# Kernel optimization log

Measured on AMD Instinct MI355X. Metric: run time of the kernel, lower is better.

The kernel has to match this reference:

```python
import jax, jax.numpy as jnp
import numpy as np

KERNEL = 5
PAD = (KERNEL - 1) // 2  # fixed_padding with dilation=1: pad_beg = pad_end = 2


def setup_inputs() -> dict:
    key = jax.random.key(0)
    kx, kw = jax.random.split(key)
    x = jax.random.normal(kx, (4, 4, 1024, 1024), dtype=jnp.float32)
    weight = jax.random.normal(kw, (4, 4, KERNEL, KERNEL), dtype=jnp.float32)
    return {"x": x, "weight": weight}


def reference(x, weight):
    """Morphological dilation2d: out[b,o,h,w] = max_{c,i,j} (x_pad[b,c,h+i,w+j] + w[o,c,i,j]).

    Equivalent to the torch unfold + broadcast-add + max over dim C*k*k, but computed
    as a fused sliding-window max-plus without materializing the im2col tensor.
    """
    B, C, H, W = x.shape
    k = weight.shape[-1]
    xp = jnp.pad(x, ((0, 0), (0, 0), (PAD, PAD), (PAD, PAD)))  # zero pad, same as F.pad
    out = None
    for i in range(k):
        for j in range(k):
            patch = xp[:, :, i:i + H, j:j + W]          # (B, C, H, W)
            w_ij = weight[:, :, i, j]                    # (O, C)
            # max over in_channels of (x + w) for this tap
            val = jnp.max(patch[:, None] + w_ij[None, :, :, None, None], axis=2)  # (B, O, H, W)
            out = val if out is None else jnp.maximum(out, val)
    return out
```

## Files before the change

kernel.cpp:

```cpp
#include <hip/hip_runtime.h>


constexpr int Himg = 1024, Wimg = 1024, Cin = 4, Cout = 4, Kn = 5;
constexpr int TH = 8, TW = 128;
constexpr int LR = TH + 4;
constexpr int LC = TW + 8;
constexpr int LC4 = LC / 4;

typedef float v2f __attribute__((ext_vector_type(2)));

__global__ void reorg_w(const float* __restrict__ w, float* __restrict__ wt) {
  int idx = threadIdx.x;
  if (idx < Cout * Cin * Kn * Kn) {
    int o  = idx / (Cin * Kn * Kn);
    int r  = idx % (Cin * Kn * Kn);
    int c  = r / (Kn * Kn);
    int r2 = r % (Kn * Kn);
    int i  = r2 / Kn, j = r2 % Kn;
    wt[((c * Kn + i) * Kn + j) * Cout + o] = w[idx];
  }
}

__device__ __forceinline__ float max5(float a, float b, float c, float d, float e) {
  return fmaxf(fmaxf(a, b), fmaxf(c, fmaxf(d, e)));
}

template <bool TRANS>
__global__ __launch_bounds__(256) void morph(const float* __restrict__ x,
                                             const float* __restrict__ wt,
                                             float* __restrict__ out) {
  __shared__ __align__(16) float xs[Cin][LR][LC];
  const int tid = threadIdx.x;
  const int tile_w0 = blockIdx.x * TW;
  const int tile_r0 = blockIdx.y * TH;
  const int b = blockIdx.z;

  for (int idx = tid; idx < Cin * LR * LC4; idx += 256) {
    const int c   = idx / (LR * LC4);
    const int rem = idx - c * (LR * LC4);
    const int row = rem / LC4;
    const int ch  = rem - row * LC4;
    const int gr  = tile_r0 - 2 + row;
    const int gc  = tile_w0 - 4 + ch * 4;
    float4 v = make_float4(0.f, 0.f, 0.f, 0.f);
    if ((unsigned)gr < (unsigned)Himg) {
      const float* src = x + ((size_t)(b * Cin + c) * Himg + gr) * Wimg;
      if (gc >= 0 && gc <= Wimg - 4) {
        v = *(const float4*)(src + gc);
      } else {
        if ((unsigned)(gc + 0) < (unsigned)Wimg) v.x = src[gc + 0];
        if ((unsigned)(gc + 1) < (unsigned)Wimg) v.y = src[gc + 1];
        if ((unsigned)(gc + 2) < (unsigned)Wimg) v.z = src[gc + 2];
        if ((unsigned)(gc + 3) < (unsigned)Wimg) v.w = src[gc + 3];
      }
    }
    *(float4*)&xs[c][row][ch * 4] = v;
  }
  __syncthreads();

  const int tx = tid & 31;
  const int ty = tid >> 5;

  float acc[Cout][4];
#pragma unroll
  for (int o = 0; o < Cout; ++o)
#pragma unroll
    for (int p = 0; p < 4; ++p) acc[o][p] = -3.4e38f;

#define ACC_O(O, WA)                                                                     \
  do {                                                                                   \
    v2f p01[5], p23[5];                                                                  \
    _Pragma("unroll") for (int j = 0; j < 5; ++j) {                                      \
      v2f wb = {WA[j], WA[j]};                                                           \
      v2f a2 = {win[2 + j], win[3 + j]};                                                 \
      v2f b2 = {win[4 + j], win[5 + j]};                                                 \
      p01[j] = a2 + wb;                                                                  \
      p23[j] = b2 + wb;                                                                  \
    }                                                                                    \
    acc[O][0] = fmaxf(acc[O][0], max5(p01[0].x, p01[1].x, p01[2].x, p01[3].x, p01[4].x)); \
    acc[O][1] = fmaxf(acc[O][1], max5(p01[0].y, p01[1].y, p01[2].y, p01[3].y, p01[4].y)); \
    acc[O][2] = fmaxf(acc[O][2], max5(p23[0].x, p23[1].x, p23[2].x, p23[3].x, p23[4].x)); \
    acc[O][3] = fmaxf(acc[O][3], max5(p23[0].y, p23[1].y, p23[2].y, p23[3].y, p23[4].y)); \
  } while (0)

#pragma unroll 1
  for (int c = 0; c < Cin; ++c) {
#pragma unroll
    for (int i = 0; i < Kn; ++i) {
      const float* rowp = &xs[c][ty + i][tx * 4];
      float4 q0 = *(const float4*)(rowp);
      float4 q1 = *(const float4*)(rowp + 4);
      float4 q2 = *(const float4*)(rowp + 8);
      float win[12] = {q0.x, q0.y, q0.z, q0.w, q1.x, q1.y, q1.z, q1.w,
                       q2.x, q2.y, q2.z, q2.w};

      float wo0[5], wo1[5], wo2[5], wo3[5];
      if (TRANS) {
        const float4* wq = (const float4*)wt + (c * Kn + i) * Kn;
#pragma unroll
        for (int j = 0; j < Kn; ++j) {
          float4 wv = wq[j];
          wo0[j] = wv.x; wo1[j] = wv.y; wo2[j] = wv.z; wo3[j] = wv.w;
        }
      } else {
#pragma unroll
        for (int j = 0; j < Kn; ++j) {
          wo0[j] = wt[((0 * Cin + c) * Kn + i) * Kn + j];
          wo1[j] = wt[((1 * Cin + c) * Kn + i) * Kn + j];
          wo2[j] = wt[((2 * Cin + c) * Kn + i) * Kn + j];
          wo3[j] = wt[((3 * Cin + c) * Kn + i) * Kn + j];
        }
      }

      ACC_O(0, wo0);
      ACC_O(1, wo1);
      ACC_O(2, wo2);
      ACC_O(3, wo3);
    }
  }
#undef ACC_O

  const int r = tile_r0 + ty;
  const int gc0 = tile_w0 + tx * 4;
#pragma unroll
  for (int o = 0; o < Cout; ++o) {
    float4 res = make_float4(acc[o][0], acc[o][1], acc[o][2], acc[o][3]);
    *(float4*)&out[((size_t)(b * Cout + o) * Himg + r) * Wimg + gc0] = res;
  }
}

extern "C" void kernel_launch(void* const* d_in, const int* in_sizes, int n_in,
                              void* d_out, int out_size, void* d_ws, size_t ws_size,
                              hipStream_t stream) {
  const float* x = (const float*)d_in[0];
  const float* w = (const float*)d_in[1];
  float* out = (float*)d_out;

  dim3 grid(Wimg / TW, Himg / TH, 4);

  if (ws_size >= sizeof(float) * Cout * Cin * Kn * Kn) {
    float* wt = (float*)d_ws;
    reorg_w<<<dim3(1), dim3(512), 0, stream>>>(w, wt);
    morph<true><<<grid, dim3(256), 0, stream>>>(x, wt, out);
  } else {
    morph<false><<<grid, dim3(256), 0, stream>>>(x, w, out);
  }
}
```

Before: 154.3 us.

## Double-buffer channel tiles in LDS with register prefetch and packed v2f max-plus

Instead of loading all four input channels into LDS at once, the kernel stages one channel at a time in a double buffer and prefetches the next channel into registers while computing the current one. The tile grows to 16 rows, and each thread now computes 8 outputs split into interleaved pairs so the adds run as packed v2f operations. Weights are pre-duplicated into pairs and read through the constant address space. The goal is to overlap global loads with compute, cut LDS footprint and raise arithmetic density, at the cost of more syncs and strided LDS reads that may cause bank conflicts.

```diff
diff --git a/kernel.cpp b/kernel.cpp
--- a/kernel.cpp
+++ b/kernel.cpp
@@ -2,14 +2,16 @@
 
 
 constexpr int Himg = 1024, Wimg = 1024, Cin = 4, Cout = 4, Kn = 5;
-constexpr int TH = 8, TW = 128;
+constexpr int TH = 16, TW = 128;
 constexpr int LR = TH + 4;
-constexpr int LC = TW + 8;
-constexpr int LC4 = LC / 4;
+constexpr int LCU = TW + 12;
+constexpr int LC = 164;
+constexpr int NCH = LR * (LCU / 4);
 
 typedef float v2f __attribute__((ext_vector_type(2)));
+typedef const float __attribute__((address_space(4))) cfloat;
 
-__global__ void reorg_w(const float* __restrict__ w, float* __restrict__ wt) {
+__global__ void reorg_w(const float* __restrict__ w, float* __restrict__ wt2) {
   int idx = threadIdx.x;
   if (idx < Cout * Cin * Kn * Kn) {
     int o  = idx / (Cin * Kn * Kn);
@@ -17,115 +19,142 @@
     int c  = r / (Kn * Kn);
     int r2 = r % (Kn * Kn);
     int i  = r2 / Kn, j = r2 % Kn;
-    wt[((c * Kn + i) * Kn + j) * Cout + o] = w[idx];
+    float v = w[idx];
+    int dst = (((c * Kn + i) * Cout + o) * Kn + j) * 2;
+    wt2[dst + 0] = v;
+    wt2[dst + 1] = v;
   }
 }
 
-__device__ __forceinline__ float max5(float a, float b, float c, float d, float e) {
-  return fmaxf(fmaxf(a, b), fmaxf(c, fmaxf(d, e)));
-}
+template <bool FAST>
+__global__ __launch_bounds__(256) void morph(const float* __restrict__ x,
+                                             const float* __restrict__ wt2,
+                                             const float* __restrict__ wraw,
+                                             float* __restrict__ out) {
+  __shared__ __align__(16) float xs[2][LR][LC];
+  const int tid = threadIdx.x;
+  const int bw = blockIdx.x * TW;
+  const int br = blockIdx.y * TH;
+  const int b  = blockIdx.z;
+  const int tx = tid & 15;
+  const int ty = tid >> 4;
 
-template <bool TRANS>
-__global__ __launch_bounds__(256) void morph(const float* __restrict__ x,
-                                             const float* __restrict__ wt,
-                                             float* __restrict__ out) {
-  __shared__ __align__(16) float xs[Cin][LR][LC];
-  const int tid = threadIdx.x;
-  const int tile_w0 = blockIdx.x * TW;
-  const int tile_r0 = blockIdx.y * TH;
-  const int b = blockIdx.z;
+  int rowk[3], gck[3];
+  bool act[3];
+#pragma unroll
+  for (int k = 0; k < 3; ++k) {
+    int idx = tid + k * 256;
+    act[k] = idx < NCH;
+    int row = idx / 35;
+    int ch  = idx - row * 35;
+    rowk[k] = row;
+    gck[k]  = bw - 4 + ch * 4;
+  }
+  const bool interior = (bw > 0) && (bw < Wimg - TW) && (br > 0) && (br < Himg - TH);
 
-  for (int idx = tid; idx < Cin * LR * LC4; idx += 256) {
-    const int c   = idx / (LR * LC4);
-    const int rem = idx - c * (LR * LC4);
-    const int row = rem / LC4;
-    const int ch  = rem - row * LC4;
-    const int gr  = tile_r0 - 2 + row;
-    const int gc  = tile_w0 - 4 + ch * 4;
-    float4 v = make_float4(0.f, 0.f, 0.f, 0.f);
-    if ((unsigned)gr < (unsigned)Himg) {
-      const float* src = x + ((size_t)(b * Cin + c) * Himg + gr) * Wimg;
-      if (gc >= 0 && gc <= Wimg - 4) {
-        v = *(const float4*)(src + gc);
-      } else {
-        if ((unsigned)(gc + 0) < (unsigned)Wimg) v.x = src[gc + 0];
-        if ((unsigned)(gc + 1) < (unsigned)Wimg) v.y = src[gc + 1];
-        if ((unsigned)(gc + 2) < (unsigned)Wimg) v.z = src[gc + 2];
-        if ((unsigned)(gc + 3) < (unsigned)Wimg) v.w = src[gc + 3];
+  float4 pre[3];
+  auto ld = [&](int c) {
+#pragma unroll
+    for (int k = 0; k < 3; ++k) {
+      float4 v = make_float4(0.f, 0.f, 0.f, 0.f);
+      if (act[k]) {
+        const int gr = br - 2 + rowk[k];
+        const int gc = gck[k];
+        const float* src = x + ((size_t)(b * Cin + c) * Himg + gr) * Wimg;
+        if (interior) {
+          v = *(const float4*)(src + gc);
+        } else if ((unsigned)gr < (unsigned)Himg) {
+          if (gc >= 0 && gc <= Wimg - 4) {
+            v = *(const float4*)(src + gc);
+          } else {
+            if ((unsigned)(gc + 0) < (unsigned)Wimg) v.x = src[gc + 0];
+            if ((unsigned)(gc + 1) < (unsigned)Wimg) v.y = src[gc + 1];
+            if ((unsigned)(gc + 2) < (unsigned)Wimg) v.z = src[gc + 2];
+            if ((unsigned)(gc + 3) < (unsigned)Wimg) v.w = src[gc + 3];
+          }
+        }
       }
+      pre[k] = v;
     }
-    *(float4*)&xs[c][row][ch * 4] = v;
-  }
-  __syncthreads();
+  };
+  auto st = [&](int buf) {
+#pragma unroll
+    for (int k = 0; k < 3; ++k) {
+      if (act[k]) *(float4*)&xs[buf][rowk[k]][(gck[k] - (bw - 4))] = pre[k];
+    }
+  };
 
-  const int tx = tid & 31;
-  const int ty = tid >> 5;
-
-  float acc[Cout][4];
+  v2f acc[Cout][4];
 #pragma unroll
   for (int o = 0; o < Cout; ++o)
 #pragma unroll
-    for (int p = 0; p < 4; ++p) acc[o][p] = -3.4e38f;
+    for (int m = 0; m < 4; ++m) acc[o][m] = (v2f){-3.4e38f, -3.4e38f};
 
-#define ACC_O(O, WA)                                                                     \
-  do {                                                                                   \
-    v2f p01[5], p23[5];                                                                  \
-    _Pragma("unroll") for (int j = 0; j < 5; ++j) {                                      \
-      v2f wb = {WA[j], WA[j]};                                                           \
-      v2f a2 = {win[2 + j], win[3 + j]};                                                 \
-      v2f b2 = {win[4 + j], win[5 + j]};                                                 \
-      p01[j] = a2 + wb;                                                                  \
-      p23[j] = b2 + wb;                                                                  \
-    }                                                                                    \
-    acc[O][0] = fmaxf(acc[O][0], max5(p01[0].x, p01[1].x, p01[2].x, p01[3].x, p01[4].x)); \
-    acc[O][1] = fmaxf(acc[O][1], max5(p01[0].y, p01[1].y, p01[2].y, p01[3].y, p01[4].y)); \
-    acc[O][2] = fmaxf(acc[O][2], max5(p23[0].x, p23[1].x, p23[2].x, p23[3].x, p23[4].x)); \
-    acc[O][3] = fmaxf(acc[O][3], max5(p23[0].y, p23[1].y, p23[2].y, p23[3].y, p23[4].y)); \
-  } while (0)
+  cfloat* cw = (cfloat*)wt2;
+
+  ld(0);
+  st(0);
+  __syncthreads();
 
 #pragma unroll 1
   for (int c = 0; c < Cin; ++c) {
+    const int buf = c & 1;
+    if (c < Cin - 1) ld(c + 1);
+
 #pragma unroll
     for (int i = 0; i < Kn; ++i) {
-      const float* rowp = &xs[c][ty + i][tx * 4];
-      float4 q0 = *(const float4*)(rowp);
-      float4 q1 = *(const float4*)(rowp + 4);
-      float4 q2 = *(const float4*)(rowp + 8);
-      float win[12] = {q0.x, q0.y, q0.z, q0.w, q1.x, q1.y, q1.z, q1.w,
-                       q2.x, q2.y, q2.z, q2.w};
-
-      float wo0[5], wo1[5], wo2[5], wo3[5];
-      if (TRANS) {
-        const float4* wq = (const float4*)wt + (c * Kn + i) * Kn;
+      const float* rowp = &xs[buf][ty + i][tx * 8];
+      v2f D[9];
+#pragma unroll
+      for (int s = 0; s < 9; ++s) {
+        v2f d; d.x = rowp[s + 2]; d.y = rowp[s + 6];
+        D[s] = d;
+      }
+#pragma unroll
+      for (int o = 0; o < Cout; ++o) {
+        v2f wv[Kn];
 #pragma unroll
         for (int j = 0; j < Kn; ++j) {
-          float4 wv = wq[j];
-          wo0[j] = wv.x; wo1[j] = wv.y; wo2[j] = wv.z; wo3[j] = wv.w;
+          if (FAST) {
+            const int widx = ((((c * Kn + i) * Cout + o) * Kn) + j) * 2;
+            v2f w2; w2.x = cw[widx]; w2.y = cw[widx + 1];
+            wv[j] = w2;
+          } else {
+            const float s0 = wraw[((o * Cin + c) * Kn + i) * Kn + j];
+            v2f w2; w2.x = s0; w2.y = s0;
+            wv[j] = w2;
+          }
         }
-      } else {
 #pragma unroll
-        for (int j = 0; j < Kn; ++j) {
-          wo0[j] = wt[((0 * Cin + c) * Kn + i) * Kn + j];
-          wo1[j] = wt[((1 * Cin + c) * Kn + i) * Kn + j];
-          wo2[j] = wt[((2 * Cin + c) * Kn + i) * Kn + j];
-          wo3[j] = wt[((3 * Cin + c) * Kn + i) * Kn + j];
+        for (int m = 0; m < 4; ++m) {
+          v2f v0 = D[m + 0] + wv[0];
+          v2f v1 = D[m + 1] + wv[1];
+          v2f v2_ = D[m + 2] + wv[2];
+          v2f v3 = D[m + 3] + wv[3];
+          v2f v4 = D[m + 4] + wv[4];
+          v2f a = acc[o][m], t1, t2;
+          t1.x = fmaxf(fmaxf(v0.x, v1.x), v2_.x);
+          t1.y = fmaxf(fmaxf(v0.y, v1.y), v2_.y);
+          t2.x = fmaxf(fmaxf(v3.x, v4.x), a.x);
+          t2.y = fmaxf(fmaxf(v3.y, v4.y), a.y);
+          a.x = fmaxf(t1.x, t2.x);
+          a.y = fmaxf(t1.y, t2.y);
+          acc[o][m] = a;
         }
       }
+    }
+    if (c < Cin - 1) st(buf ^ 1);
+    __syncthreads();
+  }
 
-      ACC_O(0, wo0);
-      ACC_O(1, wo1);
-      ACC_O(2, wo2);
-      ACC_O(3, wo3);
-    }
-  }
-#undef ACC_O
-
-  const int r = tile_r0 + ty;
-  const int gc0 = tile_w0 + tx * 4;
+  const int h = br + ty;
 #pragma unroll
   for (int o = 0; o < Cout; ++o) {
-    float4 res = make_float4(acc[o][0], acc[o][1], acc[o][2], acc[o][3]);
-    *(float4*)&out[((size_t)(b * Cout + o) * Himg + r) * Wimg + gc0] = res;
+    const size_t obase = ((size_t)(b * Cout + o) * Himg + h) * Wimg + bw + tx * 8;
+    float4 lo = make_float4(acc[o][0].x, acc[o][1].x, acc[o][2].x, acc[o][3].x);
+    float4 hi = make_float4(acc[o][0].y, acc[o][1].y, acc[o][2].y, acc[o][3].y);
+    *(float4*)&out[obase + 0] = lo;
+    *(float4*)&out[obase + 4] = hi;
   }
 }
 
@@ -138,11 +167,11 @@
 
   dim3 grid(Wimg / TW, Himg / TH, 4);
 
-  if (ws_size >= sizeof(float) * Cout * Cin * Kn * Kn) {
-    float* wt = (float*)d_ws;
-    reorg_w<<<dim3(1), dim3(512), 0, stream>>>(w, wt);
-    morph<true><<<grid, dim3(256), 0, stream>>>(x, wt, out);
+  if (ws_size >= sizeof(float) * 2 * Cout * Cin * Kn * Kn) {
+    float* wt2 = (float*)d_ws;
+    reorg_w<<<dim3(1), dim3(512), 0, stream>>>(w, wt2);
+    morph<true><<<grid, dim3(256), 0, stream>>>(x, wt2, w, out);
   } else {
-    morph<false><<<grid, dim3(256), 0, stream>>>(x, w, out);
+    morph<false><<<grid, dim3(256), 0, stream>>>(x, nullptr, w, out);
   }
 }
```

After: 197.3 us. +27.9%, slower.
